# Optimization experiments

Measured on AMD Instinct MI355X. Metric: run time of the kernel, lower is better.

Reference implementation:

```python
import jax, jax.numpy as jnp
import numpy as np

BATCH = 8192
IN_F = 1024
OUT_F = 1024
GRID = 5
K = 3            # spline order (degree)
SCALE = 1.0      # scale_spline


def setup_inputs() -> dict:
    key = jax.random.key(0)
    k1, k2, k3 = jax.random.split(key, 3)
    x = jax.random.normal(k1, (BATCH, IN_F), dtype=jnp.float32)
    # kaiming_uniform_(a=sqrt(5)) on (out,in) -> U(-1/sqrt(in), 1/sqrt(in))
    bound = 1.0 / np.sqrt(IN_F)
    base_weight = jax.random.uniform(k2, (OUT_F, IN_F), jnp.float32, -bound, bound)
    # normal(mean=0, std=0.1), shape (out, in, grid_size + spline_order)
    spline_weight = 0.1 * jax.random.normal(k3, (OUT_F, IN_F, GRID + K), dtype=jnp.float32)
    # extended knot vector: uniform grid on [-1,1] with spacing h, padded by K knots each side
    h = 2.0 / GRID
    knots = jnp.arange(-K, GRID + K + 1, dtype=jnp.float32) * h - 1.0  # (GRID+2K+1,)
    grid = jnp.tile(knots[None, :], (IN_F, 1))                          # (in, GRID+2K+1)
    return {"x": x, "base_weight": base_weight, "spline_weight": spline_weight, "grid": grid}


def _b_splines(x, grid, k):
    # x: (B, in), grid: (in, G+2k+1) -> basis: (B, in, G+k)
    xe = x[..., None]  # (B, in, 1)
    basis = ((xe >= grid[:, :-1]) & (xe < grid[:, 1:])).astype(x.dtype)  # degree-0, (B,in,G+2k)
    for p in range(1, k + 1):  # Cox-de Boor recursion, degree p
        left = (xe - grid[:, :-(p + 1)]) / (grid[:, p:-1] - grid[:, :-(p + 1)]) * basis[..., :-1]
        right = (grid[:, (p + 1):] - xe) / (grid[:, (p + 1):] - grid[:, 1:-p]) * basis[..., 1:]
        basis = left + right
    return basis


def reference(x, base_weight, spline_weight, grid):
    base = x @ base_weight.T                                   # (B, out)
    basis = _b_splines(x, grid, K)                             # (B, in, G+K)
    spline = jnp.einsum('bic,oic->bo', basis, spline_weight)   # (B, out)
    return base + SCALE * spline
```

## Files before the change

kernel.cpp:

```cpp
#include <hip/hip_runtime.h>


#define BATCH 8192
#define IN_F  1024
#define OUT_F 1024
#define NC    9
#define KAUG  (IN_F * NC)

typedef float  f32x4  __attribute__((ext_vector_type(4)));
typedef __bf16 bf16x8 __attribute__((ext_vector_type(8)));
typedef unsigned short u16;
typedef u16 u16x8 __attribute__((ext_vector_type(8)));

__device__ __forceinline__ u16 f2bf(float f) {
  unsigned int u = __builtin_bit_cast(unsigned int, f);
  u += 0x7FFFu + ((u >> 16) & 1u);
  return (u16)(u >> 16);
}

#define KT(j) ((float)((j) - 3) * 0.4f - 1.0f)

__device__ __forceinline__ void bspline8(float x, float bas[11]) {
#pragma unroll
  for (int j = 0; j < 11; ++j)
    bas[j] = (x >= KT(j) && x < KT(j + 1)) ? 1.0f : 0.0f;
#pragma unroll
  for (int p = 1; p <= 3; ++p) {
#pragma unroll
    for (int j = 0; j < 11 - p; ++j) {
      bas[j] = (x - KT(j)) * (1.0f / (KT(j + p) - KT(j))) * bas[j]
             + (KT(j + p + 1) - x) * (1.0f / (KT(j + p + 1) - KT(j + 1))) * bas[j + 1];
    }
  }
}

__global__ __launch_bounds__(256) void build_AW(const float* __restrict__ X,
                                                const float* __restrict__ BW,
                                                const float* __restrict__ SW,
                                                u16* __restrict__ Aa,
                                                u16* __restrict__ Wa) {
  const int idx = blockIdx.x * 256 + threadIdx.x;
  if (idx < BATCH * 128) {
    const int b  = idx >> 7;
    const int i0 = (idx & 127) << 3;
    const float4* xp = (const float4*)(X + (size_t)b * IN_F + i0);
    float4 xa = xp[0], xb = xp[1];
    float xs[8] = {xa.x, xa.y, xa.z, xa.w, xb.x, xb.y, xb.z, xb.w};
    u16x8 out[9];
#pragma unroll
    for (int e = 0; e < 8; ++e) {
      const float x = xs[e];
      out[0][e] = f2bf(x);
      float bas[11];
      bspline8(x, bas);
#pragma unroll
      for (int c = 0; c < 8; ++c) out[c + 1][e] = f2bf(bas[c]);
    }
    u16* row = Aa + (size_t)b * KAUG + i0;
#pragma unroll
    for (int c = 0; c < 9; ++c) *(u16x8*)(row + c * IN_F) = out[c];
  } else {
    const int wdx = idx - BATCH * 128;
    const int o  = wdx >> 7;
    const int i0 = (wdx & 127) << 3;
    u16x8 out[9];
    const float4* bp = (const float4*)(BW + (size_t)o * IN_F + i0);
    float4 b0 = bp[0], b1 = bp[1];
    float bs[8] = {b0.x, b0.y, b0.z, b0.w, b1.x, b1.y, b1.z, b1.w};
#pragma unroll
    for (int e = 0; e < 8; ++e) out[0][e] = f2bf(bs[e]);
    const float4* sp = (const float4*)(SW + ((size_t)o * IN_F + i0) * 8);
#pragma unroll
    for (int e = 0; e < 8; ++e) {
      float4 s0 = sp[e * 2], s1 = sp[e * 2 + 1];
      out[1][e] = f2bf(s0.x);
      out[2][e] = f2bf(s0.y);
      out[3][e] = f2bf(s0.z);
      out[4][e] = f2bf(s0.w);
      out[5][e] = f2bf(s1.x);
      out[6][e] = f2bf(s1.y);
      out[7][e] = f2bf(s1.z);
      out[8][e] = f2bf(s1.w);
    }
    u16* row = Wa + (size_t)o * KAUG + i0;
#pragma unroll
    for (int c = 0; c < 9; ++c) *(u16x8*)(row + c * IN_F) = out[c];
  }
}

#define BM 128
#define BN 128
#define BKP 32
#define NP  4

__device__ __forceinline__ void async16(const u16* g, u16* l) {
  __builtin_amdgcn_global_load_lds(
      (const __attribute__((address_space(1))) u16*)g,
      (__attribute__((address_space(3))) u16*)l,
      16, 0, 0);
}

__global__ __launch_bounds__(256) void gemm_bt(
    const u16* __restrict__ A,
    const u16* __restrict__ B,
    float* __restrict__ C) {
  constexpr int N = OUT_F, K = KAUG;
  __shared__ u16 As[NP][BM * BKP];
  __shared__ u16 Bs[NP][BN * BKP];

  const int tid  = threadIdx.x;
  const int bm   = blockIdx.x;
  const int bn   = blockIdx.y;
  const int lane = tid & 63;
  const int wave = tid >> 6;
  const int wm   = wave >> 1;
  const int wn   = wave & 1;

  const int srow = tid >> 2;
  const int scol = (tid & 3) * 8;
  const u16* Ag = A + (size_t)(bm * BM + srow) * K + scol;
  const u16* Bg = B + (size_t)(bn * BN + srow) * K + scol;

  const int frow = lane & 15;
  const int fk   = (lane >> 4) * 8;

  f32x4 acc[4][4] = {};

  for (int k0 = 0; k0 < K; k0 += NP * BKP) {
#pragma unroll
    for (int p = 0; p < NP; ++p) {
      async16(Ag + k0 + p * BKP,                  &As[p][tid * 8]);
      async16(Ag + (size_t)64 * K + k0 + p * BKP, &As[p][tid * 8 + 64 * BKP]);
      async16(Bg + k0 + p * BKP,                  &Bs[p][tid * 8]);
      async16(Bg + (size_t)64 * K + k0 + p * BKP, &Bs[p][tid * 8 + 64 * BKP]);
    }
    __syncthreads();

#pragma unroll
    for (int p = 0; p < NP; ++p) {
      bf16x8 af[4], bfr[4];
#pragma unroll
      for (int t = 0; t < 4; ++t) {
        af[t]  = *(const bf16x8*)(&As[p][(wm * 64 + t * 16 + frow) * BKP + fk]);
        bfr[t] = *(const bf16x8*)(&Bs[p][(wn * 64 + t * 16 + frow) * BKP + fk]);
      }
#pragma unroll
      for (int i = 0; i < 4; ++i)
#pragma unroll
        for (int j = 0; j < 4; ++j)
          acc[i][j] = __builtin_amdgcn_mfma_f32_16x16x32_bf16(af[i], bfr[j], acc[i][j], 0, 0, 0);
    }
    __syncthreads();
  }

  const int r0 = bm * BM + wm * 64 + (lane >> 4) * 4;
  const int c0 = bn * BN + wn * 64 + (lane & 15);
#pragma unroll
  for (int i = 0; i < 4; ++i)
#pragma unroll
    for (int j = 0; j < 4; ++j) {
      float* cp = C + (size_t)(r0 + i * 16) * N + (c0 + j * 16);
#pragma unroll
      for (int r = 0; r < 4; ++r) cp[(size_t)r * N] = acc[i][j][r];
    }
}

extern "C" void kernel_launch(void* const* d_in, const int* in_sizes, int n_in,
                              void* d_out, int out_size, void* d_ws, size_t ws_size,
                              hipStream_t stream) {
  const float* x  = (const float*)d_in[0];
  const float* bw = (const float*)d_in[1];
  const float* sw = (const float*)d_in[2];
  float* out = (float*)d_out;

  u16* Aaug = (u16*)d_ws;
  u16* Waug = Aaug + (size_t)BATCH * KAUG;

  build_AW<<<dim3((BATCH + OUT_F) * 128 / 256), 256, 0, stream>>>(x, bw, sw, Aaug, Waug);
  gemm_bt<<<dim3(BATCH / BM, OUT_F / BN), 256, 0, stream>>>(Aaug, Waug, out);
}
```

Before: 302.7 us.

## Rewrite GEMM with triple-buffered async pipeline, swizzled LDS, and larger tiles

The GEMM is restructured to use 256x128 tiles with 512 threads and BK=64. Async global-to-LDS loads run through a three-stage ring buffer with explicit vmcnt waits, and prefetches are interleaved with MFMA phases under s_setprio. An XOR swizzle on the LDS layout avoids bank conflicts, and block IDs are remapped so neighbouring blocks share tiles in cache. The aim is to hide memory latency and raise MFMA utilisation, at the cost of more LDS (about 144KB), many barriers, and fragile hand scheduling.

```diff
diff --git a/kernel.cpp b/kernel.cpp
--- a/kernel.cpp
+++ b/kernel.cpp
@@ -88,10 +88,10 @@
   }
 }
 
-#define BM 128
+#define BM 256
 #define BN 128
-#define BKP 32
-#define NP  4
+#define BK 64
+#define NT (KAUG / BK)
 
 __device__ __forceinline__ void async16(const u16* g, u16* l) {
   __builtin_amdgcn_global_load_lds(
@@ -100,61 +100,138 @@
       16, 0, 0);
 }
 
-__global__ __launch_bounds__(256) void gemm_bt(
+__global__ __launch_bounds__(512) void gemm_bt(
     const u16* __restrict__ A,
     const u16* __restrict__ B,
     float* __restrict__ C) {
   constexpr int N = OUT_F, K = KAUG;
-  __shared__ u16 As[NP][BM * BKP];
-  __shared__ u16 Bs[NP][BN * BKP];
-
-  const int tid  = threadIdx.x;
-  const int bm   = blockIdx.x;
-  const int bn   = blockIdx.y;
+  __shared__ __align__(16) u16 sm[3][24576];
+
+  const int tid = threadIdx.x;
+
+  const int bid = blockIdx.x;
+  const int wg  = (bid & 7) * 32 + (bid >> 3);
+  const int bm  = wg >> 3;
+  const int bn  = wg & 7;
+
   const int lane = tid & 63;
-  const int wave = tid >> 6;
-  const int wm   = wave >> 1;
-  const int wn   = wave & 1;
-
-  const int srow = tid >> 2;
-  const int scol = (tid & 3) * 8;
-  const u16* Ag = A + (size_t)(bm * BM + srow) * K + scol;
-  const u16* Bg = B + (size_t)(bn * BN + srow) * K + scol;
-
-  const int frow = lane & 15;
-  const int fk   = (lane >> 4) * 8;
+  const int wid  = tid >> 6;
+  const int wm   = wid >> 1;
+  const int wn   = wid & 1;
+  const int fr   = lane & 15;
+  const int hi   = lane >> 4;
+
+  const int ak0 = ((hi      ^ (fr & 7)) << 3);
+  const int ak1 = (((4 | hi) ^ (fr & 7)) << 3);
+  int arow[4], brow[4];
+#pragma unroll
+  for (int m = 0; m < 4; ++m) arow[m] = (wm * 64 + m * 16 + fr) * 64;
+#pragma unroll
+  for (int n = 0; n < 4; ++n) brow[n] = 16384 + (wn * 64 + n * 16 + fr) * 64;
+
+  const int trow = tid >> 3;
+  const int gsrc = (tid & 7) ^ (trow & 7);
+  const u16* Asrc = A + (size_t)(bm * BM + trow) * K + gsrc * 8;
+  const u16* Bsrc = B + (size_t)(bn * BN + trow) * K + gsrc * 8;
+
+#pragma unroll
+  for (int tt = 0; tt < 2; ++tt) {
+    u16* dA = &sm[tt][0] + tid * 8;
+    u16* dB = &sm[tt][16384] + tid * 8;
+    const size_t kg = (size_t)tt * BK;
+    async16(Asrc + kg, dA);
+    async16(Asrc + (size_t)64  * K + kg, dA + 4096);
+    async16(Asrc + (size_t)128 * K + kg, dA + 8192);
+    async16(Asrc + (size_t)192 * K + kg, dA + 12288);
+    async16(Bsrc + kg, dB);
+    async16(Bsrc + (size_t)64  * K + kg, dB + 4096);
+  }
 
   f32x4 acc[4][4] = {};
 
-  for (int k0 = 0; k0 < K; k0 += NP * BKP) {
-#pragma unroll
-    for (int p = 0; p < NP; ++p) {
-      async16(Ag + k0 + p * BKP,                  &As[p][tid * 8]);
-      async16(Ag + (size_t)64 * K + k0 + p * BKP, &As[p][tid * 8 + 64 * BKP]);
-      async16(Bg + k0 + p * BKP,                  &Bs[p][tid * 8]);
-      async16(Bg + (size_t)64 * K + k0 + p * BKP, &Bs[p][tid * 8 + 64 * BKP]);
-    }
-    __syncthreads();
-
-#pragma unroll
-    for (int p = 0; p < NP; ++p) {
-      bf16x8 af[4], bfr[4];
-#pragma unroll
-      for (int t = 0; t < 4; ++t) {
-        af[t]  = *(const bf16x8*)(&As[p][(wm * 64 + t * 16 + frow) * BKP + fk]);
-        bfr[t] = *(const bf16x8*)(&Bs[p][(wn * 64 + t * 16 + frow) * BKP + fk]);
-      }
-#pragma unroll
-      for (int i = 0; i < 4; ++i)
-#pragma unroll
-        for (int j = 0; j < 4; ++j)
-          acc[i][j] = __builtin_amdgcn_mfma_f32_16x16x32_bf16(af[i], bfr[j], acc[i][j], 0, 0, 0);
-    }
-    __syncthreads();
-  }
-
-  const int r0 = bm * BM + wm * 64 + (lane >> 4) * 4;
-  const int c0 = bn * BN + wn * 64 + (lane & 15);
+  for (int t = 0; t < NT; ++t) {
+    const int cur = t % 3;
+    const int nxt = (t + 2) % 3;
+    const bool pf = (t + 2) < NT;
+    const size_t kg = (size_t)(t + 2) * BK;
+    const u16* s0 = &sm[cur][0];
+    u16* dA = &sm[nxt][0] + tid * 8;
+    u16* dB = &sm[nxt][16384] + tid * 8;
+
+    if (t < NT - 1) asm volatile("s_waitcnt vmcnt(6)" ::: "memory");
+    else            asm volatile("s_waitcnt vmcnt(0)" ::: "memory");
+    __builtin_amdgcn_s_barrier();
+    __builtin_amdgcn_sched_barrier(0);
+
+    bf16x8 bf[4], a0, a1;
+#pragma unroll
+    for (int n = 0; n < 4; ++n) bf[n] = *(const bf16x8*)(s0 + brow[n] + ak0);
+    a0 = *(const bf16x8*)(s0 + arow[0] + ak0);
+    a1 = *(const bf16x8*)(s0 + arow[1] + ak0);
+    if (pf) {
+      async16(Asrc + kg, dA);
+      async16(Asrc + (size_t)64 * K + kg, dA + 4096);
+    }
+    __builtin_amdgcn_s_barrier();
+    __builtin_amdgcn_s_setprio(1);
+#pragma unroll
+    for (int n = 0; n < 4; ++n)
+      acc[0][n] = __builtin_amdgcn_mfma_f32_16x16x32_bf16(a0, bf[n], acc[0][n], 0, 0, 0);
+#pragma unroll
+    for (int n = 0; n < 4; ++n)
+      acc[1][n] = __builtin_amdgcn_mfma_f32_16x16x32_bf16(a1, bf[n], acc[1][n], 0, 0, 0);
+    __builtin_amdgcn_s_setprio(0);
+    __builtin_amdgcn_s_barrier();
+    a0 = *(const bf16x8*)(s0 + arow[2] + ak0);
+    a1 = *(const bf16x8*)(s0 + arow[3] + ak0);
+    if (pf) {
+      async16(Asrc + (size_t)128 * K + kg, dA + 8192);
+      async16(Asrc + (size_t)192 * K + kg, dA + 12288);
+    }
+    __builtin_amdgcn_s_barrier();
+    __builtin_amdgcn_s_setprio(1);
+#pragma unroll
+    for (int n = 0; n < 4; ++n)
+      acc[2][n] = __builtin_amdgcn_mfma_f32_16x16x32_bf16(a0, bf[n], acc[2][n], 0, 0, 0);
+#pragma unroll
+    for (int n = 0; n < 4; ++n)
+      acc[3][n] = __builtin_amdgcn_mfma_f32_16x16x32_bf16(a1, bf[n], acc[3][n], 0, 0, 0);
+    __builtin_amdgcn_s_setprio(0);
+    __builtin_amdgcn_s_barrier();
+#pragma unroll
+    for (int n = 0; n < 4; ++n) bf[n] = *(const bf16x8*)(s0 + brow[n] + ak1);
+    a0 = *(const bf16x8*)(s0 + arow[0] + ak1);
+    a1 = *(const bf16x8*)(s0 + arow[1] + ak1);
+    if (pf) {
+      async16(Bsrc + kg, dB);
+      async16(Bsrc + (size_t)64 * K + kg, dB + 4096);
+    }
+    __builtin_amdgcn_s_barrier();
+    __builtin_amdgcn_s_setprio(1);
+#pragma unroll
+    for (int n = 0; n < 4; ++n)
+      acc[0][n] = __builtin_amdgcn_mfma_f32_16x16x32_bf16(a0, bf[n], acc[0][n], 0, 0, 0);
+#pragma unroll
+    for (int n = 0; n < 4; ++n)
+      acc[1][n] = __builtin_amdgcn_mfma_f32_16x16x32_bf16(a1, bf[n], acc[1][n], 0, 0, 0);
+    __builtin_amdgcn_s_setprio(0);
+    __builtin_amdgcn_s_barrier();
+    a0 = *(const bf16x8*)(s0 + arow[2] + ak1);
+    a1 = *(const bf16x8*)(s0 + arow[3] + ak1);
+    __builtin_amdgcn_s_barrier();
+    __builtin_amdgcn_s_setprio(1);
+#pragma unroll
+    for (int n = 0; n < 4; ++n)
+      acc[2][n] = __builtin_amdgcn_mfma_f32_16x16x32_bf16(a0, bf[n], acc[2][n], 0, 0, 0);
+#pragma unroll
+    for (int n = 0; n < 4; ++n)
+      acc[3][n] = __builtin_amdgcn_mfma_f32_16x16x32_bf16(a1, bf[n], acc[3][n], 0, 0, 0);
+    __builtin_amdgcn_s_setprio(0);
+    __builtin_amdgcn_s_barrier();
+  }
+
+  const int r0 = bm * BM + wm * 64 + hi * 4;
+  const int c0 = bn * BN + wn * 64 + fr;
 #pragma unroll
   for (int i = 0; i < 4; ++i)
 #pragma unroll
@@ -177,5 +254,5 @@
   u16* Waug = Aaug + (size_t)BATCH * KAUG;
 
   build_AW<<<dim3((BATCH + OUT_F) * 128 / 256), 256, 0, stream>>>(x, bw, sw, Aaug, Waug);
-  gemm_bt<<<dim3(BATCH / BM, OUT_F / BN), 256, 0, stream>>>(Aaug, Waug, out);
-}
+  gemm_bt<<<dim3(BATCH / BM * (OUT_F / BN)), 512, 0, stream>>>(Aaug, Waug, out);
+}
```

After: 279.7 us. 7.6% less time.
